# Optimization experiments

Hardware: AMD Instinct MI355X
Metric: run time of the kernel (lower is better)

## Reference

```python
import jax, jax.numpy as jnp
import numpy as np

B, LQ, LK, DQ, DKEY, DV = 8, 2048, 2048, 1024, 1024, 1024
MASK_NEG = -1e6  # d2l masked_softmax fill value


def setup_inputs() -> dict:
    key = jax.random.key(0)
    kq, kk, kv, kl, kw = jax.random.split(key, 5)
    queries = jax.random.normal(kq, (B, LQ, DQ), dtype=jnp.float32)
    keys = jax.random.normal(kk, (B, LK, DKEY), dtype=jnp.float32)
    values = jax.random.normal(kv, (B, LK, DV), dtype=jnp.float32)
    valid_lens = jax.random.randint(kl, (B,), 1, LK + 1)
    W_q = jax.random.normal(kw, (DQ, DKEY), dtype=jnp.float32) / np.sqrt(DQ)
    return {"queries": queries, "keys": keys, "values": values,
            "valid_lens": valid_lens, "W_q": W_q}


def reference(queries, keys, values, valid_lens, W_q):
    # Q projection: LazyLinear(key_dim, bias=False)
    q = jnp.einsum("bqd,dk->bqk", queries, W_q)          # [B, LQ, DKEY]
    d = q.shape[-1]
    scores = jnp.einsum("bqk,bsk->bqs", q, keys) / jnp.sqrt(jnp.asarray(d, q.dtype))
    # masked_softmax: positions >= valid_len set to -1e6 before softmax
    mask = jnp.arange(scores.shape[-1])[None, None, :] < valid_lens[:, None, None]
    scores = jnp.where(mask, scores, MASK_NEG)
    attn = jax.nn.softmax(scores, axis=-1)               # [B, LQ, LK]
    # dropout p=0.0 (eval) -> identity
    return jnp.einsum("bqs,bsv->bqv", attn, values)      # [B, LQ, DV]
```

## Files before the change

kernel.cpp:

```cpp
#include <hip/hip_runtime.h>
#include <cstdint>
#include <cstddef>

#define B_   8
#define LQ_  2048
#define LK_  2048

typedef __attribute__((ext_vector_type(8))) __bf16 bf16x8;
typedef __attribute__((ext_vector_type(4))) float f32x4;
typedef __attribute__((ext_vector_type(8))) unsigned short ushortx8;

__device__ __forceinline__ unsigned short f2bf(float f) {
  unsigned u = __builtin_bit_cast(unsigned, f);
  u = u + 0x7fffu + ((u >> 16) & 1u);
  return (unsigned short)(u >> 16);
}
__device__ __forceinline__ float bf2f(unsigned short h) {
  unsigned u = ((unsigned)h) << 16;
  return __builtin_bit_cast(float, u);
}

__device__ __forceinline__ void gld_lds16(const void* g, void* l) {
  __builtin_amdgcn_global_load_lds((__attribute__((address_space(1))) void*)(void*)g,
                                   (__attribute__((address_space(3))) void*)l, 16, 0, 0);
}

__global__ __launch_bounds__(256) void cast2_bf16_kernel(
    const float* __restrict__ in0, unsigned short* __restrict__ out0,
    const float* __restrict__ in1, unsigned short* __restrict__ out1,
    size_t half_blocks) {
  const float* in = blockIdx.x < half_blocks ? in0 : in1;
  unsigned short* out = blockIdx.x < half_blocks ? out0 : out1;
  size_t bb = blockIdx.x < half_blocks ? blockIdx.x : blockIdx.x - half_blocks;
  size_t i = (bb * 256 + threadIdx.x) * 8;
  float4 a = *(const float4*)(in + i);
  float4 b = *(const float4*)(in + i + 4);
  ushortx8 o;
  o[0] = f2bf(a.x); o[1] = f2bf(a.y); o[2] = f2bf(a.z); o[3] = f2bf(a.w);
  o[4] = f2bf(b.x); o[5] = f2bf(b.y); o[6] = f2bf(b.z); o[7] = f2bf(b.w);
  *(ushortx8*)(out + i) = o;
}

__global__ __launch_bounds__(256) void transpose_cast_kernel(
    const float* __restrict__ in, unsigned short* __restrict__ out,
    int R, int C, long in_bstride, long out_bstride) {
  __shared__ float t[32][33];
  const float* inb = in + (size_t)blockIdx.z * in_bstride;
  unsigned short* outb = out + (size_t)blockIdx.z * out_bstride;
  int c0 = blockIdx.x * 32, r0 = blockIdx.y * 32;
  int tx = threadIdx.x, ty = threadIdx.y;
#pragma unroll
  for (int k = 0; k < 4; ++k) {
    int r = ty + k * 8;
    t[r][tx] = inb[(size_t)(r0 + r) * C + c0 + tx];
  }
  __syncthreads();
#pragma unroll
  for (int k = 0; k < 4; ++k) {
    int c = ty + k * 8;
    outb[(size_t)(c0 + c) * R + r0 + tx] = f2bf(t[tx][c]);
  }
}

template <int OUTM, int SKIPN, int CLAMPK>
__global__ __launch_bounds__(512, 2) void gemm256_kernel(
    const unsigned short* __restrict__ A, const unsigned short* __restrict__ B,
    void* __restrict__ Cp, int M, int N, int K,
    long a_bstride, long b_bstride, long c_bstride, float scale,
    const int* __restrict__ vlp) {
  __shared__ unsigned short lds[4][2][128 * 64];

  const int tid = threadIdx.x;
  const int wid = tid >> 6;
  const int lane = tid & 63;
  const int lane15 = lane & 15;
  const int lhalf = lane >> 4;

  const int nt = (int)((blockIdx.x + 2 * blockIdx.z) & (gridDim.x - 1));
  const int m0 = blockIdx.y * 256;
  const int n0 = nt * 256;

  int vl = K;
  if constexpr (SKIPN || CLAMPK) vl = vlp[blockIdx.z];
  if constexpr (SKIPN) {
    if (n0 >= vl) return;
  }
  int kEnd = K;
  if constexpr (CLAMPK) {
    int ke = (vl + 63) & ~63;
    kEnd = ke < K ? ke : K;
  }
  const int nKt = kEnd >> 5;

  const unsigned short* Ab = A + (size_t)blockIdx.z * a_bstride;
  const unsigned short* Bb = B + (size_t)blockIdx.z * b_bstride;

  int srowA[2], srowB[2], scol[2], sdst[2];
#pragma unroll
  for (int j = 0; j < 2; ++j) {
    int blk = (wid * 2 + j) * 64 + lane;
    int p = blk >> 3, q = blk & 7;
    int c = q ^ (p & 7);
    int r = 2 * p + (c >> 2);
    scol[j] = (c & 3) * 8;
    srowA[j] = m0 + r;
    srowB[j] = n0 + r;
    sdst[j] = blk * 8;
  }

  const int om = (wid >> 2) * 128;
  const int on = (wid & 3) * 64;
  const int swz8 = ((((lane15 & 1) << 2) + lhalf) ^ ((lane15 >> 1) & 7)) << 3;
  const int aBase = ((om >> 1) + (lane15 >> 1)) * 64 + swz8;
  const int bBase = ((on >> 1) + (lane15 >> 1)) * 64 + swz8;

  f32x4 acc[8][4];
#pragma unroll
  for (int f = 0; f < 8; ++f)
#pragma unroll
    for (int g = 0; g < 4; ++g) acc[f][g] = (f32x4){0.f, 0.f, 0.f, 0.f};

#pragma unroll
  for (int j = 0; j < 2; ++j)
    gld_lds16(Ab + (size_t)srowA[j] * K + scol[j], &lds[0][0][sdst[j]]);
#pragma unroll
  for (int j = 0; j < 2; ++j)
    gld_lds16(Bb + (size_t)srowB[j] * K + scol[j], &lds[0][1][sdst[j]]);
#pragma unroll
  for (int j = 0; j < 2; ++j)
    gld_lds16(Ab + (size_t)srowA[j] * K + (32 + scol[j]), &lds[1][0][sdst[j]]);
#pragma unroll
  for (int j = 0; j < 2; ++j)
    gld_lds16(Bb + (size_t)srowB[j] * K + (32 + scol[j]), &lds[1][1][sdst[j]]);
  asm volatile("s_waitcnt vmcnt(4)" ::: "memory");
  __builtin_amdgcn_s_barrier();

  for (int t = 0; t < nKt; ++t) {
    const unsigned short* lA = &lds[t & 3][0][0];
    const unsigned short* lB = &lds[t & 3][1][0];
    const bool st = (t + 2) < nKt;
    const int nb = (t + 2) & 3;
    const int kc = (t + 2) * 32;

    bf16x8 a0[4], b0[4];
#pragma unroll
    for (int f = 0; f < 4; ++f) a0[f] = *(const bf16x8*)&lA[aBase + f * 512];
#pragma unroll
    for (int g = 0; g < 4; ++g) b0[g] = *(const bf16x8*)&lB[bBase + g * 512];
    if (st) {
#pragma unroll
      for (int j = 0; j < 2; ++j)
        gld_lds16(Ab + (size_t)srowA[j] * K + (kc + scol[j]), &lds[nb][0][sdst[j]]);
    }
    __builtin_amdgcn_s_barrier();
    asm volatile("s_waitcnt lgkmcnt(0)" ::: "memory");
    __builtin_amdgcn_sched_barrier(0);
    __builtin_amdgcn_s_setprio(1);
#pragma unroll
    for (int f = 0; f < 4; ++f)
#pragma unroll
      for (int g = 0; g < 4; ++g)
        acc[f][g] = __builtin_amdgcn_mfma_f32_16x16x32_bf16(a0[f], b0[g], acc[f][g], 0, 0, 0);
    __builtin_amdgcn_s_setprio(0);
    __builtin_amdgcn_s_barrier();

    bf16x8 a1[4];
#pragma unroll
    for (int f = 0; f < 4; ++f) a1[f] = *(const bf16x8*)&lA[aBase + (f + 4) * 512];
    if (st) {
#pragma unroll
      for (int j = 0; j < 2; ++j)
        gld_lds16(Bb + (size_t)srowB[j] * K + (kc + scol[j]), &lds[nb][1][sdst[j]]);
    }
    __builtin_amdgcn_s_barrier();
    asm volatile("s_waitcnt lgkmcnt(0)" ::: "memory");
    __builtin_amdgcn_sched_barrier(0);
    __builtin_amdgcn_s_setprio(1);
#pragma unroll
    for (int f = 0; f < 4; ++f)
#pragma unroll
      for (int g = 0; g < 4; ++g)
        acc[f + 4][g] = __builtin_amdgcn_mfma_f32_16x16x32_bf16(a1[f], b0[g], acc[f + 4][g], 0, 0, 0);
    __builtin_amdgcn_s_setprio(0);
    if (st)
      asm volatile("s_waitcnt vmcnt(4)" ::: "memory");
    else
      asm volatile("s_waitcnt vmcnt(0)" ::: "memory");
    __builtin_amdgcn_s_barrier();
  }

  const size_t boffC = (size_t)blockIdx.z * c_bstride;
#pragma unroll
  for (int f = 0; f < 8; ++f) {
    int row = m0 + om + f * 16 + lhalf * 4;
#pragma unroll
    for (int g = 0; g < 4; ++g) {
      int col = n0 + on + g * 16 + lane15;
#pragma unroll
      for (int r = 0; r < 4; ++r) {
        float v = acc[f][g][r];
        if constexpr (OUTM == 0) {
          ((unsigned short*)Cp + boffC)[(size_t)(row + r) * N + col] = f2bf(v);
        } else if constexpr (OUTM == 1) {
          ((unsigned short*)Cp + boffC)[(size_t)(row + r) * N + col] = f2bf(v * scale);
        } else {
          ((float*)Cp + boffC)[(size_t)(row + r) * N + col] = v;
        }
      }
    }
  }
}

__global__ __launch_bounds__(256) void softmax_kernel(unsigned short* __restrict__ scores,
                                                      const int* __restrict__ valid_lens) {
  const int row = blockIdx.x;
  const int b = row >> 11;
  const int vl = valid_lens[b];
  const int kEnd = (vl + 63) & ~63;
  unsigned short* rp = scores + (size_t)row * LK_;
  const int tid = threadIdx.x;
  const int wid = tid >> 6, lane = tid & 63;
  __shared__ float sred[4];

  const int cb = tid * 8;
  const bool act = cb < kEnd;
  ushortx8 h = {};
  if (act) h = *(const ushortx8*)(rp + cb);
  float x[8];
#pragma unroll
  for (int t = 0; t < 8; ++t) x[t] = bf2f(h[t]);

  float m = -3.4e38f;
#pragma unroll
  for (int t = 0; t < 8; ++t)
    if (cb + t < vl) m = fmaxf(m, x[t]);
#pragma unroll
  for (int off = 32; off >= 1; off >>= 1) m = fmaxf(m, __shfl_xor(m, off));
  if (lane == 0) sred[wid] = m;
  __syncthreads();
  m = fmaxf(fmaxf(sred[0], sred[1]), fmaxf(sred[2], sred[3]));
  __syncthreads();

  float e[8];
  float s = 0.f;
#pragma unroll
  for (int t = 0; t < 8; ++t) {
    e[t] = (cb + t < vl) ? __expf(x[t] - m) : 0.f;
    s += e[t];
  }
#pragma unroll
  for (int off = 32; off >= 1; off >>= 1) s += __shfl_xor(s, off);
  if (lane == 0) sred[wid] = s;
  __syncthreads();
  s = sred[0] + sred[1] + sred[2] + sred[3];
  float inv = 1.f / s;

  if (act) {
    ushortx8 o;
#pragma unroll
    for (int t = 0; t < 8; ++t) o[t] = f2bf(e[t] * inv);
    *(ushortx8*)(rp + cb) = o;
  }
}

extern "C" void kernel_launch(void* const* d_in, const int* in_sizes, int n_in,
                              void* d_out, int out_size, void* d_ws, size_t ws_size,
                              hipStream_t stream) {
  const float* queries = (const float*)d_in[0];
  const float* keys = (const float*)d_in[1];
  const float* values = (const float*)d_in[2];
  const int* valid_lens = (const int*)d_in[3];
  const float* W_q = (const float*)d_in[4];
  float* out = (float*)d_out;

  unsigned short* ws = (unsigned short*)d_ws;
  const size_t M1 = (size_t)1024 * 1024;
  unsigned short* q_bf = ws;
  unsigned short* scores = ws + 16 * M1;
  unsigned short* qry_bf = scores;
  unsigned short* valsT = ws + 48 * M1;
  unsigned short* wqT = ws + 64 * M1;
  unsigned short* keys_bf = ws + 65 * M1;

  cast2_bf16_kernel<<<dim3(16384), 256, 0, stream>>>(queries, qry_bf, keys, keys_bf, 8192);
  transpose_cast_kernel<<<dim3(32, 32, 1), dim3(32, 8), 0, stream>>>(
      W_q, wqT, 1024, 1024, 0, 0);
  transpose_cast_kernel<<<dim3(32, 64, 8), dim3(32, 8), 0, stream>>>(
      values, valsT, 2048, 1024, (long)2048 * 1024, (long)1024 * 2048);
  gemm256_kernel<0, 0, 0><<<dim3(4, 64, 1), 512, 0, stream>>>(
      qry_bf, wqT, q_bf, 16384, 1024, 1024, 0, 0, 0, 1.f, nullptr);
  gemm256_kernel<1, 1, 0><<<dim3(8, 8, 8), 512, 0, stream>>>(
      q_bf, keys_bf, scores, 2048, 2048, 1024,
      (long)2048 * 1024, (long)2048 * 1024, (long)2048 * 2048, 0.03125f, valid_lens);
  softmax_kernel<<<dim3(B_ * LQ_), 256, 0, stream>>>(scores, valid_lens);
  gemm256_kernel<2, 0, 1><<<dim3(4, 8, 8), 512, 0, stream>>>(
      scores, valsT, out, 2048, 1024, 2048,
      (long)2048 * 2048, (long)1024 * 2048, (long)2048 * 1024, 1.f, valid_lens);
}
```

Measured before the change: 406.7 us.

## Reassociate Q projection onto keys, skip padded rows, deepen GEMM prefetch

Instead of projecting all queries by W_q, the scores GEMM now uses keys projected by W_q (K·W_qᵀ, applied as q·(K W_q)ᵀ), and only key rows below the padded valid length are cast and projected. W_q is cast without transposing, since the GEMM B layout makes the transpose unnecessary. The values transpose also skips rows past the clamped K range. The GEMM software pipeline now prefetches three stages ahead instead of two, with adjusted vmcnt waits. Together these are meant to cut projection FLOPs and memory traffic, at the cost of more in-flight loads and a changed rounding order.

```diff
diff --git a/kernel.cpp b/kernel.cpp
--- a/kernel.cpp
+++ b/kernel.cpp
@@ -25,14 +25,28 @@
                                    (__attribute__((address_space(3))) void*)l, 16, 0, 0);
 }
 
-__global__ __launch_bounds__(256) void cast2_bf16_kernel(
-    const float* __restrict__ in0, unsigned short* __restrict__ out0,
-    const float* __restrict__ in1, unsigned short* __restrict__ out1,
-    size_t half_blocks) {
-  const float* in = blockIdx.x < half_blocks ? in0 : in1;
-  unsigned short* out = blockIdx.x < half_blocks ? out0 : out1;
-  size_t bb = blockIdx.x < half_blocks ? blockIdx.x : blockIdx.x - half_blocks;
-  size_t i = (bb * 256 + threadIdx.x) * 8;
+__global__ __launch_bounds__(256) void cast3_bf16_kernel(
+    const float* __restrict__ q, unsigned short* __restrict__ qo,
+    const float* __restrict__ k, unsigned short* __restrict__ ko,
+    const float* __restrict__ w, unsigned short* __restrict__ wo,
+    const int* __restrict__ vlp) {
+  int bb = (int)blockIdx.x;
+  const float* in;
+  unsigned short* out;
+  if (bb < 8192) {
+    in = q; out = qo;
+  } else if (bb < 16384) {
+    bb -= 8192;
+    in = k; out = ko;
+    int batch = bb >> 10;
+    int row = (bb & 1023) * 2;
+    int vl = vlp[batch];
+    if (row >= ((vl + 255) & ~255)) return;
+  } else {
+    bb -= 16384;
+    in = w; out = wo;
+  }
+  size_t i = ((size_t)bb * 256 + threadIdx.x) * 8;
   float4 a = *(const float4*)(in + i);
   float4 b = *(const float4*)(in + i + 4);
   ushortx8 o;
@@ -43,11 +57,16 @@
 
 __global__ __launch_bounds__(256) void transpose_cast_kernel(
     const float* __restrict__ in, unsigned short* __restrict__ out,
-    int R, int C, long in_bstride, long out_bstride) {
+    int R, int C, long in_bstride, long out_bstride, const int* __restrict__ vlp) {
   __shared__ float t[32][33];
+  int r0 = blockIdx.y * 32;
+  if (vlp) {
+    int kEnd = (vlp[blockIdx.z] + 63) & ~63;
+    if (r0 >= kEnd) return;
+  }
   const float* inb = in + (size_t)blockIdx.z * in_bstride;
   unsigned short* outb = out + (size_t)blockIdx.z * out_bstride;
-  int c0 = blockIdx.x * 32, r0 = blockIdx.y * 32;
+  int c0 = blockIdx.x * 32;
   int tx = threadIdx.x, ty = threadIdx.y;
 #pragma unroll
   for (int k = 0; k < 4; ++k) {
@@ -62,7 +81,7 @@
   }
 }
 
-template <int OUTM, int SKIPN, int CLAMPK>
+template <int OUTM, int SKIPN, int SKIPM, int CLAMPK>
 __global__ __launch_bounds__(512, 2) void gemm256_kernel(
     const unsigned short* __restrict__ A, const unsigned short* __restrict__ B,
     void* __restrict__ Cp, int M, int N, int K,
@@ -81,9 +100,12 @@
   const int n0 = nt * 256;
 
   int vl = K;
-  if constexpr (SKIPN || CLAMPK) vl = vlp[blockIdx.z];
+  if constexpr (SKIPN || SKIPM || CLAMPK) vl = vlp[blockIdx.z];
   if constexpr (SKIPN) {
     if (n0 >= vl) return;
+  }
+  if constexpr (SKIPM) {
+    if (m0 >= vl) return;
   }
   int kEnd = K;
   if constexpr (CLAMPK) {
@@ -132,15 +154,25 @@
 #pragma unroll
   for (int j = 0; j < 2; ++j)
     gld_lds16(Bb + (size_t)srowB[j] * K + (32 + scol[j]), &lds[1][1][sdst[j]]);
-  asm volatile("s_waitcnt vmcnt(4)" ::: "memory");
+  if (nKt > 2) {
+#pragma unroll
+    for (int j = 0; j < 2; ++j)
+      gld_lds16(Ab + (size_t)srowA[j] * K + (64 + scol[j]), &lds[2][0][sdst[j]]);
+#pragma unroll
+    for (int j = 0; j < 2; ++j)
+      gld_lds16(Bb + (size_t)srowB[j] * K + (64 + scol[j]), &lds[2][1][sdst[j]]);
+    asm volatile("s_waitcnt vmcnt(8)" ::: "memory");
+  } else {
+    asm volatile("s_waitcnt vmcnt(4)" ::: "memory");
+  }
   __builtin_amdgcn_s_barrier();
 
   for (int t = 0; t < nKt; ++t) {
     const unsigned short* lA = &lds[t & 3][0][0];
     const unsigned short* lB = &lds[t & 3][1][0];
-    const bool st = (t + 2) < nKt;
-    const int nb = (t + 2) & 3;
-    const int kc = (t + 2) * 32;
+    const bool st = (t + 3) < nKt;
+    const int nb = (t + 3) & 3;
+    const int kc = (t + 3) * 32;
 
     bf16x8 a0[4], b0[4];
 #pragma unroll
@@ -182,10 +214,16 @@
       for (int g = 0; g < 4; ++g)
         acc[f + 4][g] = __builtin_amdgcn_mfma_f32_16x16x32_bf16(a1[f], b0[g], acc[f + 4][g], 0, 0, 0);
     __builtin_amdgcn_s_setprio(0);
-    if (st)
-      asm volatile("s_waitcnt vmcnt(4)" ::: "memory");
-    else
-      asm volatile("s_waitcnt vmcnt(0)" ::: "memory");
+    {
+      int hi = nKt < t + 4 ? nKt : t + 4;
+      int pend = hi - (t + 2);
+      if (pend >= 2)
+        asm volatile("s_waitcnt vmcnt(8)" ::: "memory");
+      else if (pend == 1)
+        asm volatile("s_waitcnt vmcnt(4)" ::: "memory");
+      else
+        asm volatile("s_waitcnt vmcnt(0)" ::: "memory");
+    }
     __builtin_amdgcn_s_barrier();
   }
 
@@ -277,23 +315,23 @@
   const size_t M1 = (size_t)1024 * 1024;
   unsigned short* q_bf = ws;
   unsigned short* scores = ws + 16 * M1;
-  unsigned short* qry_bf = scores;
-  unsigned short* valsT = ws + 48 * M1;
-  unsigned short* wqT = ws + 64 * M1;
+  unsigned short* keysP = ws + 48 * M1;
+  unsigned short* valsT = keysP;
+  unsigned short* w_bf = ws + 64 * M1;
   unsigned short* keys_bf = ws + 65 * M1;
 
-  cast2_bf16_kernel<<<dim3(16384), 256, 0, stream>>>(queries, qry_bf, keys, keys_bf, 8192);
-  transpose_cast_kernel<<<dim3(32, 32, 1), dim3(32, 8), 0, stream>>>(
-      W_q, wqT, 1024, 1024, 0, 0);
+  cast3_bf16_kernel<<<dim3(16896), 256, 0, stream>>>(
+      queries, q_bf, keys, keys_bf, W_q, w_bf, valid_lens);
+  gemm256_kernel<0, 0, 1, 0><<<dim3(4, 8, 8), 512, 0, stream>>>(
+      keys_bf, w_bf, keysP, 2048, 1024, 1024,
+      (long)2048 * 1024, 0, (long)2048 * 1024, 1.f, valid_lens);
+  gemm256_kernel<1, 1, 0, 0><<<dim3(8, 8, 8), 512, 0, stream>>>(
+      q_bf, keysP, scores, 2048, 2048, 1024,
+      (long)2048 * 1024, (long)2048 * 1024, (long)2048 * 2048, 0.03125f, valid_lens);
   transpose_cast_kernel<<<dim3(32, 64, 8), dim3(32, 8), 0, stream>>>(
-      values, valsT, 2048, 1024, (long)2048 * 1024, (long)1024 * 2048);
-  gemm256_kernel<0, 0, 0><<<dim3(4, 64, 1), 512, 0, stream>>>(
-      qry_bf, wqT, q_bf, 16384, 1024, 1024, 0, 0, 0, 1.f, nullptr);
-  gemm256_kernel<1, 1, 0><<<dim3(8, 8, 8), 512, 0, stream>>>(
-      q_bf, keys_bf, scores, 2048, 2048, 1024,
-      (long)2048 * 1024, (long)2048 * 1024, (long)2048 * 2048, 0.03125f, valid_lens);
+      values, valsT, 2048, 1024, (long)2048 * 1024, (long)1024 * 2048, valid_lens);
   softmax_kernel<<<dim3(B_ * LQ_), 256, 0, stream>>>(scores, valid_lens);
-  gemm256_kernel<2, 0, 1><<<dim3(4, 8, 8), 512, 0, stream>>>(
+  gemm256_kernel<2, 0, 0, 1><<<dim3(4, 8, 8), 512, 0, stream>>>(
       scores, valsT, out, 2048, 1024, 2048,
       (long)2048 * 2048, (long)1024 * 2048, (long)2048 * 1024, 1.f, valid_lens);
 }
```

After: 381.3 us. 6.3% less time.
